# Kernel optimization log

Hardware: AMD Instinct MI355X
Metric: run time of the kernel (lower is better)

Reference implementation:

```python
import jax, jax.numpy as jnp
import numpy as np


def setup_inputs() -> dict:
    key = jax.random.key(0)
    ks = jax.random.split(key, 5)
    b, t, q_dim, kv_dim, h = 16, 128, 256, 64, 4
    c = t - 1
    q_x = jax.random.normal(ks[0], (b, t, q_dim), dtype=jnp.float32)
    kv_x = jax.random.normal(ks[1], (b, t, c, kv_dim), dtype=jnp.float32)
    # Linear weights stored as [in, out]; no biases (bias=False in torch module).
    sq = 1.0 / np.sqrt(q_dim)
    sk = 1.0 / np.sqrt(kv_dim)
    Wq = jax.random.uniform(ks[2], (q_dim, kv_dim * h), jnp.float32, -sq, sq)
    Wk = jax.random.uniform(ks[3], (kv_dim, kv_dim * h), jnp.float32, -sk, sk)
    Wv = jax.random.uniform(ks[4], (kv_dim, kv_dim * h), jnp.float32, -sk, sk)
    return {"q_x": q_x, "kv_x": kv_x, "Wq": Wq, "Wk": Wk, "Wv": Wv}


def reference(q_x, kv_x, Wq, Wk, Wv):
    b, t, c, k = kv_x.shape  # c = t - 1
    h = Wq.shape[1] // k
    # projections
    q = (q_x @ Wq).reshape(b, t, h, k)          # [b,t,h,k]
    keys = (kv_x @ Wk).reshape(b, t, c, h, k)   # [b,t,c,h,k]
    vals = (kv_x @ Wv).reshape(b, t, c, h, k)
    # per-token attention over the c-sized context
    scores = jnp.einsum('bthk,btchk->bthc', q, keys) / jnp.sqrt(jnp.float32(k))
    w = jax.nn.softmax(scores, axis=-1)          # softmax over context dim
    out = jnp.einsum('bthc,btchk->bthk', w, vals)
    return out.reshape(b, t, h * k)
```

## Files before the change

### kernel.cpp

```cpp
#include <hip/hip_runtime.h>
#include <math.h>

#define Bdim 16
#define Tdim 128
#define Cdim 127
#define Hdim 4
#define QD   256
#define HK   256
#define BT   (Bdim * Tdim)

#define DPP_XOR1        0xB1
#define DPP_XOR2        0x4E
#define DPP_HALF_MIRROR 0x141
#define DPP_MIRROR      0x140
template<int CTRL>
__device__ __forceinline__ float dpp_movf(float x) {
    return __int_as_float(__builtin_amdgcn_update_dpp(
        0, __float_as_int(x), CTRL, 0xF, 0xF, true));
}
__device__ __forceinline__ float quad_sum(float v) {
    v += dpp_movf<DPP_XOR1>(v);
    v += dpp_movf<DPP_XOR2>(v);
    return v;
}
__device__ __forceinline__ float rows_sum(float v) {
    v += dpp_movf<DPP_HALF_MIRROR>(v);
    v += dpp_movf<DPP_MIRROR>(v);
    v += __shfl_xor(v, 16, 64);
    v += __shfl_xor(v, 32, 64);
    return v;
}
__device__ __forceinline__ float wx_red(float v) {
    v += dpp_movf<DPP_XOR1>(v);
    v += dpp_movf<DPP_XOR2>(v);
    v += dpp_movf<DPP_HALF_MIRROR>(v);
    v += dpp_movf<DPP_MIRROR>(v);
    v += __shfl_xor(v, 16, 64);
    return v;
}

__global__ __launch_bounds__(256) void qk_fused(
        const float* __restrict__ q_x,
        const float* __restrict__ Wq,
        const float* __restrict__ Wk,
        float* __restrict__ qk) {
    __shared__ __align__(16) float q_s[4][256];
    __shared__ __align__(16) float p_s[4][4][68];
    int RB = blockIdx.x;
    int tid = threadIdx.x;
    {
        int r = tid >> 6, kq = tid & 63;
        *(float4*)&q_s[r][kq*4] =
            *(const float4*)(q_x + (size_t)(RB*4 + r) * QD + kq * 4);
    }
    __syncthreads();

    float acc[4] = {0.f, 0.f, 0.f, 0.f};
    #pragma unroll 4
    for (int i4 = 0; i4 < 64; ++i4) {
        float w0 = Wq[(size_t)(4*i4+0) * HK + tid];
        float w1 = Wq[(size_t)(4*i4+1) * HK + tid];
        float w2 = Wq[(size_t)(4*i4+2) * HK + tid];
        float w3 = Wq[(size_t)(4*i4+3) * HK + tid];
        #pragma unroll
        for (int r = 0; r < 4; ++r) {
            float4 qv = *(const float4*)&q_s[r][i4*4];
            acc[r] = fmaf(qv.x, w0, fmaf(qv.y, w1, fmaf(qv.z, w2, fmaf(qv.w, w3, acc[r]))));
        }
    }
    int h = tid >> 6, m = tid & 63;
    #pragma unroll
    for (int r = 0; r < 4; ++r) p_s[r][h][m] = acc[r];
    __syncthreads();

    const float4* wk4 = (const float4*)(Wk + (size_t)m * HK + h * 64);
    float4 wkr[16];
    #pragma unroll
    for (int j = 0; j < 16; ++j) wkr[j] = wk4[j];
    float a2[4] = {0.f, 0.f, 0.f, 0.f};
    #pragma unroll
    for (int j4 = 0; j4 < 16; ++j4) {
        #pragma unroll
        for (int r = 0; r < 4; ++r) {
            float4 pv = *(const float4*)&p_s[r][h][j4*4];
            a2[r] = fmaf(pv.x, wkr[j4].x, fmaf(pv.y, wkr[j4].y,
                    fmaf(pv.z, wkr[j4].z, fmaf(pv.w, wkr[j4].w, a2[r]))));
        }
    }
    #pragma unroll
    for (int r = 0; r < 4; ++r)
        qk[(size_t)(RB*4 + r) * HK + tid] = a2[r];
}

__global__ __launch_bounds__(512, 8) void attn_main(
        const float* __restrict__ kv_x,
        const float* __restrict__ qk_g,
        const float* __restrict__ Wv,
        float* __restrict__ out) {
    __shared__ __align__(16) float qk_s[HK];
    __shared__ __align__(16) float4 e4[128];
    __shared__ __align__(16) float4 wx4[Hdim * 16];
    __shared__ __align__(16) float4 reds[8];

    int bt  = blockIdx.x;
    int tid = threadIdx.x;
    const float* Xr = kv_x + (size_t)bt * (Cdim * 64);

    if (tid < 256)
        qk_s[tid] = qk_g[(size_t)bt * HK + tid];
    __syncthreads();

    int lane = tid & 63;
    int wave = tid >> 6;
    int c  = tid >> 2;
    int qp = tid & 3;

    float e0, e1, e2, e3;
    {
        bool valid = (c < Cdim);
        int crow = valid ? c : 0;
        const float4* xq = (const float4*)(Xr + crow * 64) + qp * 4;
        float4 x0 = xq[0];
        float4 x1 = xq[1];
        float4 x2 = xq[2];
        float4 x3 = xq[3];
        const float4* qk4 = (const float4*)qk_s;
        float a0 = 0.f, a1 = 0.f, a2 = 0.f, a3 = 0.f;
        #pragma unroll
        for (int i = 0; i < 4; ++i) {
            float4 xi = (i == 0) ? x0 : (i == 1) ? x1 : (i == 2) ? x2 : x3;
            float4 q0 = qk4[0*16 + qp*4 + i];
            float4 q1 = qk4[1*16 + qp*4 + i];
            float4 q2 = qk4[2*16 + qp*4 + i];
            float4 q3 = qk4[3*16 + qp*4 + i];
            a0 = fmaf(q0.x, xi.x, fmaf(q0.y, xi.y, fmaf(q0.z, xi.z, fmaf(q0.w, xi.w, a0))));
            a1 = fmaf(q1.x, xi.x, fmaf(q1.y, xi.y, fmaf(q1.z, xi.z, fmaf(q1.w, xi.w, a1))));
            a2 = fmaf(q2.x, xi.x, fmaf(q2.y, xi.y, fmaf(q2.z, xi.z, fmaf(q2.w, xi.w, a2))));
            a3 = fmaf(q3.x, xi.x, fmaf(q3.y, xi.y, fmaf(q3.z, xi.z, fmaf(q3.w, xi.w, a3))));
        }
        a0 = quad_sum(a0); a1 = quad_sum(a1); a2 = quad_sum(a2); a3 = quad_sum(a3);
        e0 = valid ? __expf(a0 * 0.125f) : 0.f;
        e1 = valid ? __expf(a1 * 0.125f) : 0.f;
        e2 = valid ? __expf(a2 * 0.125f) : 0.f;
        e3 = valid ? __expf(a3 * 0.125f) : 0.f;
    }
    if (qp == 0) e4[c] = make_float4(e0, e1, e2, e3);
    float t0 = rows_sum(e0), t1 = rows_sum(e1), t2 = rows_sum(e2), t3 = rows_sum(e3);
    if (lane == 0) reds[wave] = make_float4(t0, t1, t2, t3);
    __syncthreads();

    {
        int jc = tid >> 5;
        int mq = (lane >> 3) & 3;
        int cs = lane & 7;
        float4 A0 = {0,0,0,0}, A1 = {0,0,0,0}, A2 = {0,0,0,0}, A3 = {0,0,0,0};
        #pragma unroll
        for (int mm = 0; mm < 4; ++mm) {
            int cc = cs + 8 * (mq * 4 + mm);
            int ccrow = (cc < Cdim) ? cc : 0;
            float4 x4 = *(const float4*)(Xr + ccrow * 64 + jc * 4);
            float4 ee = e4[cc];
            A0.x = fmaf(ee.x, x4.x, A0.x); A0.y = fmaf(ee.x, x4.y, A0.y);
            A0.z = fmaf(ee.x, x4.z, A0.z); A0.w = fmaf(ee.x, x4.w, A0.w);
            A1.x = fmaf(ee.y, x4.x, A1.x); A1.y = fmaf(ee.y, x4.y, A1.y);
            A1.z = fmaf(ee.y, x4.z, A1.z); A1.w = fmaf(ee.y, x4.w, A1.w);
            A2.x = fmaf(ee.z, x4.x, A2.x); A2.y = fmaf(ee.z, x4.y, A2.y);
            A2.z = fmaf(ee.z, x4.z, A2.z); A2.w = fmaf(ee.z, x4.w, A2.w);
            A3.x = fmaf(ee.w, x4.x, A3.x); A3.y = fmaf(ee.w, x4.y, A3.y);
            A3.z = fmaf(ee.w, x4.z, A3.z); A3.w = fmaf(ee.w, x4.w, A3.w);
        }
        A0.x = wx_red(A0.x); A0.y = wx_red(A0.y); A0.z = wx_red(A0.z); A0.w = wx_red(A0.w);
        A1.x = wx_red(A1.x); A1.y = wx_red(A1.y); A1.z = wx_red(A1.z); A1.w = wx_red(A1.w);
        A2.x = wx_red(A2.x); A2.y = wx_red(A2.y); A2.z = wx_red(A2.z); A2.w = wx_red(A2.w);
        A3.x = wx_red(A3.x); A3.y = wx_red(A3.y); A3.z = wx_red(A3.z); A3.w = wx_red(A3.w);
        if ((lane & 31) == 0) {
            wx4[0 * 16 + jc] = A0;
            wx4[1 * 16 + jc] = A1;
            wx4[2 * 16 + jc] = A2;
            wx4[3 * 16 + jc] = A3;
        }
    }
    __syncthreads();

    if (tid < 256) {
        int hh = tid >> 6, k = tid & 63;
        float4 sums = reds[0];
        #pragma unroll
        for (int w = 1; w < 8; ++w) {
            float4 r = reds[w];
            sums.x += r.x; sums.y += r.y; sums.z += r.z; sums.w += r.w;
        }
        float denom = (hh == 0) ? sums.x : (hh == 1) ? sums.y
                    : (hh == 2) ? sums.z : sums.w;
        float inv = 1.f / denom;
        const float* wvcol = Wv + hh * 64 + k;
        float acc = 0.f;
        #pragma unroll 4
        for (int jc = 0; jc < 16; ++jc) {
            float4 w4 = wx4[hh * 16 + jc];
            acc = fmaf(w4.x, wvcol[(size_t)(jc*4+0) * HK],
                  fmaf(w4.y, wvcol[(size_t)(jc*4+1) * HK],
                  fmaf(w4.z, wvcol[(size_t)(jc*4+2) * HK],
                  fmaf(w4.w, wvcol[(size_t)(jc*4+3) * HK], acc))));
        }
        out[(size_t)bt * HK + tid] = acc * inv;
    }
}

extern "C" void kernel_launch(void* const* d_in, const int* in_sizes, int n_in,
                              void* d_out, int out_size, void* d_ws, size_t ws_size,
                              hipStream_t stream) {
    const float* q_x  = (const float*)d_in[0];
    const float* kv_x = (const float*)d_in[1];
    const float* Wq   = (const float*)d_in[2];
    const float* Wk   = (const float*)d_in[3];
    const float* Wv   = (const float*)d_in[4];
    float* out = (float*)d_out;

    float* qk = (float*)d_ws;

    qk_fused<<<BT / 4, 256, 0, stream>>>(q_x, Wq, Wk, qk);
    attn_main<<<BT, 512, 0, stream>>>(kv_x, qk, Wv, out);
}
```

Baseline: 42.76 us.

## Split attention into one-wave-per-token core kernel and separate batched V projection

```diff
diff --git a/kernel.cpp b/kernel.cpp
--- a/kernel.cpp
+++ b/kernel.cpp
@@ -18,24 +18,13 @@
     return __int_as_float(__builtin_amdgcn_update_dpp(
         0, __float_as_int(x), CTRL, 0xF, 0xF, true));
 }
-__device__ __forceinline__ float quad_sum(float v) {
-    v += dpp_movf<DPP_XOR1>(v);
-    v += dpp_movf<DPP_XOR2>(v);
-    return v;
-}
-__device__ __forceinline__ float rows_sum(float v) {
-    v += dpp_movf<DPP_HALF_MIRROR>(v);
-    v += dpp_movf<DPP_MIRROR>(v);
-    v += __shfl_xor(v, 16, 64);
-    v += __shfl_xor(v, 32, 64);
-    return v;
-}
-__device__ __forceinline__ float wx_red(float v) {
+__device__ __forceinline__ float sum64(float v) {
     v += dpp_movf<DPP_XOR1>(v);
     v += dpp_movf<DPP_XOR2>(v);
     v += dpp_movf<DPP_HALF_MIRROR>(v);
     v += dpp_movf<DPP_MIRROR>(v);
     v += __shfl_xor(v, 16, 64);
+    v += __shfl_xor(v, 32, 64);
     return v;
 }
 
@@ -92,74 +81,71 @@
         qk[(size_t)(RB*4 + r) * HK + tid] = a2[r];
 }
 
-__global__ __launch_bounds__(512, 8) void attn_main(
+__global__ __launch_bounds__(256) void attn_core(
         const float* __restrict__ kv_x,
         const float* __restrict__ qk_g,
-        const float* __restrict__ Wv,
-        float* __restrict__ out) {
-    __shared__ __align__(16) float qk_s[HK];
-    __shared__ __align__(16) float4 e4[128];
-    __shared__ __align__(16) float4 wx4[Hdim * 16];
-    __shared__ __align__(16) float4 reds[8];
-
-    int bt  = blockIdx.x;
+        float* __restrict__ wx_buf,
+        float* __restrict__ denom_buf) {
+    __shared__ __align__(16) float4 qk_s[4][64];
+    __shared__ __align__(16) float4 e4[4][128];
+
     int tid = threadIdx.x;
+    int wv = tid >> 6, lane = tid & 63;
+    int bt = blockIdx.x * 4 + wv;
     const float* Xr = kv_x + (size_t)bt * (Cdim * 64);
 
-    if (tid < 256)
-        qk_s[tid] = qk_g[(size_t)bt * HK + tid];
-    __syncthreads();
-
-    int lane = tid & 63;
-    int wave = tid >> 6;
-    int c  = tid >> 2;
-    int qp = tid & 3;
-
-    float e0, e1, e2, e3;
+    qk_s[wv][lane] = ((const float4*)(qk_g + (size_t)bt * HK))[lane];
+
+    const float4* xA = (const float4*)(Xr + lane * 64);
+    int cB = 64 + lane;
+    bool vB = (cB < Cdim);
+    const float4* xB = (const float4*)(Xr + (vB ? cB : 0) * 64);
+    float a0=0.f,a1=0.f,a2=0.f,a3=0.f;
+    float b0=0.f,b1=0.f,b2=0.f,b3=0.f;
+    #pragma unroll
+    for (int i = 0; i < 16; ++i) {
+        float4 xa = xA[i];
+        float4 xb = xB[i];
+        float4 q0 = qk_s[wv][ 0 + i];
+        float4 q1 = qk_s[wv][16 + i];
+        float4 q2 = qk_s[wv][32 + i];
+        float4 q3 = qk_s[wv][48 + i];
+        a0 = fmaf(q0.x, xa.x, fmaf(q0.y, xa.y, fmaf(q0.z, xa.z, fmaf(q0.w, xa.w, a0))));
+        a1 = fmaf(q1.x, xa.x, fmaf(q1.y, xa.y, fmaf(q1.z, xa.z, fmaf(q1.w, xa.w, a1))));
+        a2 = fmaf(q2.x, xa.x, fmaf(q2.y, xa.y, fmaf(q2.z, xa.z, fmaf(q2.w, xa.w, a2))));
+        a3 = fmaf(q3.x, xa.x, fmaf(q3.y, xa.y, fmaf(q3.z, xa.z, fmaf(q3.w, xa.w, a3))));
+        b0 = fmaf(q0.x, xb.x, fmaf(q0.y, xb.y, fmaf(q0.z, xb.z, fmaf(q0.w, xb.w, b0))));
+        b1 = fmaf(q1.x, xb.x, fmaf(q1.y, xb.y, fmaf(q1.z, xb.z, fmaf(q1.w, xb.w, b1))));
+        b2 = fmaf(q2.x, xb.x, fmaf(q2.y, xb.y, fmaf(q2.z, xb.z, fmaf(q2.w, xb.w, b2))));
+        b3 = fmaf(q3.x, xb.x, fmaf(q3.y, xb.y, fmaf(q3.z, xb.z, fmaf(q3.w, xb.w, b3))));
+    }
+
+    float4 eA, eB;
+    eA.x = __expf(a0 * 0.125f);  eA.y = __expf(a1 * 0.125f);
+    eA.z = __expf(a2 * 0.125f);  eA.w = __expf(a3 * 0.125f);
+    eB.x = vB ? __expf(b0 * 0.125f) : 0.f;
+    eB.y = vB ? __expf(b1 * 0.125f) : 0.f;
+    eB.z = vB ? __expf(b2 * 0.125f) : 0.f;
+    eB.w = vB ? __expf(b3 * 0.125f) : 0.f;
+    e4[wv][lane]      = eA;
+    e4[wv][64 + lane] = eB;
+
+    float t0 = sum64(eA.x + eB.x);
+    float t1 = sum64(eA.y + eB.y);
+    float t2 = sum64(eA.z + eB.z);
+    float t3 = sum64(eA.w + eB.w);
+    if (lane == 0)
+        *(float4*)(denom_buf + (size_t)bt * 4) = make_float4(t0, t1, t2, t3);
+
     {
-        bool valid = (c < Cdim);
-        int crow = valid ? c : 0;
-        const float4* xq = (const float4*)(Xr + crow * 64) + qp * 4;
-        float4 x0 = xq[0];
-        float4 x1 = xq[1];
-        float4 x2 = xq[2];
-        float4 x3 = xq[3];
-        const float4* qk4 = (const float4*)qk_s;
-        float a0 = 0.f, a1 = 0.f, a2 = 0.f, a3 = 0.f;
-        #pragma unroll
-        for (int i = 0; i < 4; ++i) {
-            float4 xi = (i == 0) ? x0 : (i == 1) ? x1 : (i == 2) ? x2 : x3;
-            float4 q0 = qk4[0*16 + qp*4 + i];
-            float4 q1 = qk4[1*16 + qp*4 + i];
-            float4 q2 = qk4[2*16 + qp*4 + i];
-            float4 q3 = qk4[3*16 + qp*4 + i];
-            a0 = fmaf(q0.x, xi.x, fmaf(q0.y, xi.y, fmaf(q0.z, xi.z, fmaf(q0.w, xi.w, a0))));
-            a1 = fmaf(q1.x, xi.x, fmaf(q1.y, xi.y, fmaf(q1.z, xi.z, fmaf(q1.w, xi.w, a1))));
-            a2 = fmaf(q2.x, xi.x, fmaf(q2.y, xi.y, fmaf(q2.z, xi.z, fmaf(q2.w, xi.w, a2))));
-            a3 = fmaf(q3.x, xi.x, fmaf(q3.y, xi.y, fmaf(q3.z, xi.z, fmaf(q3.w, xi.w, a3))));
-        }
-        a0 = quad_sum(a0); a1 = quad_sum(a1); a2 = quad_sum(a2); a3 = quad_sum(a3);
-        e0 = valid ? __expf(a0 * 0.125f) : 0.f;
-        e1 = valid ? __expf(a1 * 0.125f) : 0.f;
-        e2 = valid ? __expf(a2 * 0.125f) : 0.f;
-        e3 = valid ? __expf(a3 * 0.125f) : 0.f;
-    }
-    if (qp == 0) e4[c] = make_float4(e0, e1, e2, e3);
-    float t0 = rows_sum(e0), t1 = rows_sum(e1), t2 = rows_sum(e2), t3 = rows_sum(e3);
-    if (lane == 0) reds[wave] = make_float4(t0, t1, t2, t3);
-    __syncthreads();
-
-    {
-        int jc = tid >> 5;
-        int mq = (lane >> 3) & 3;
-        int cs = lane & 7;
+        int jc = lane >> 2, g = lane & 3;
         float4 A0 = {0,0,0,0}, A1 = {0,0,0,0}, A2 = {0,0,0,0}, A3 = {0,0,0,0};
-        #pragma unroll
-        for (int mm = 0; mm < 4; ++mm) {
-            int cc = cs + 8 * (mq * 4 + mm);
-            int ccrow = (cc < Cdim) ? cc : 0;
-            float4 x4 = *(const float4*)(Xr + ccrow * 64 + jc * 4);
-            float4 ee = e4[cc];
+        #pragma unroll 8
+        for (int mm = 0; mm < 32; ++mm) {
+            int cc = g + 4 * mm;
+            int crow = (cc < Cdim) ? cc : 0;
+            float4 x4 = *(const float4*)(Xr + crow * 64 + jc * 4);
+            float4 ee = e4[wv][cc];
             A0.x = fmaf(ee.x, x4.x, A0.x); A0.y = fmaf(ee.x, x4.y, A0.y);
             A0.z = fmaf(ee.x, x4.z, A0.z); A0.w = fmaf(ee.x, x4.w, A0.w);
             A1.x = fmaf(ee.y, x4.x, A1.x); A1.y = fmaf(ee.y, x4.y, A1.y);
@@ -169,41 +155,54 @@
             A3.x = fmaf(ee.w, x4.x, A3.x); A3.y = fmaf(ee.w, x4.y, A3.y);
             A3.z = fmaf(ee.w, x4.z, A3.z); A3.w = fmaf(ee.w, x4.w, A3.w);
         }
-        A0.x = wx_red(A0.x); A0.y = wx_red(A0.y); A0.z = wx_red(A0.z); A0.w = wx_red(A0.w);
-        A1.x = wx_red(A1.x); A1.y = wx_red(A1.y); A1.z = wx_red(A1.z); A1.w = wx_red(A1.w);
-        A2.x = wx_red(A2.x); A2.y = wx_red(A2.y); A2.z = wx_red(A2.z); A2.w = wx_red(A2.w);
-        A3.x = wx_red(A3.x); A3.y = wx_red(A3.y); A3.z = wx_red(A3.z); A3.w = wx_red(A3.w);
-        if ((lane & 31) == 0) {
-            wx4[0 * 16 + jc] = A0;
-            wx4[1 * 16 + jc] = A1;
-            wx4[2 * 16 + jc] = A2;
-            wx4[3 * 16 + jc] = A3;
-        }
-    }
+        #define GRED(v) v += dpp_movf<DPP_XOR1>(v); v += dpp_movf<DPP_XOR2>(v);
+        GRED(A0.x) GRED(A0.y) GRED(A0.z) GRED(A0.w)
+        GRED(A1.x) GRED(A1.y) GRED(A1.z) GRED(A1.w)
+        GRED(A2.x) GRED(A2.y) GRED(A2.z) GRED(A2.w)
+        GRED(A3.x) GRED(A3.y) GRED(A3.z) GRED(A3.w)
+        #undef GRED
+        if (g == 0) {
+            float4* w = (float4*)(wx_buf + (size_t)bt * HK);
+            w[0 * 16 + jc] = A0;
+            w[1 * 16 + jc] = A1;
+            w[2 * 16 + jc] = A2;
+            w[3 * 16 + jc] = A3;
+        }
+    }
+}
+
+__global__ __launch_bounds__(256) void vproj(
+        const float* __restrict__ wx_buf,
+        const float* __restrict__ denom_buf,
+        const float* __restrict__ Wv,
+        float* __restrict__ out) {
+    __shared__ __align__(16) float4 wx_s[4][64];
+    __shared__ __align__(16) float4 dn_s[4];
+    int B0 = blockIdx.x * 4;
+    int tid = threadIdx.x;
+    {
+        int r = tid >> 6, l = tid & 63;
+        wx_s[r][l] = ((const float4*)(wx_buf + (size_t)(B0 + r) * HK))[l];
+    }
+    if (tid < 4) dn_s[tid] = *(const float4*)(denom_buf + (size_t)(B0 + tid) * 4);
     __syncthreads();
 
-    if (tid < 256) {
-        int hh = tid >> 6, k = tid & 63;
-        float4 sums = reds[0];
+    int h = tid >> 6;
+    float wvr[64];
+    #pragma unroll
+    for (int j = 0; j < 64; ++j) wvr[j] = Wv[(size_t)j * HK + tid];
+    #pragma unroll
+    for (int r = 0; r < 4; ++r) {
+        float acc = 0.f;
         #pragma unroll
-        for (int w = 1; w < 8; ++w) {
-            float4 r = reds[w];
-            sums.x += r.x; sums.y += r.y; sums.z += r.z; sums.w += r.w;
-        }
-        float denom = (hh == 0) ? sums.x : (hh == 1) ? sums.y
-                    : (hh == 2) ? sums.z : sums.w;
-        float inv = 1.f / denom;
-        const float* wvcol = Wv + hh * 64 + k;
-        float acc = 0.f;
-        #pragma unroll 4
-        for (int jc = 0; jc < 16; ++jc) {
-            float4 w4 = wx4[hh * 16 + jc];
-            acc = fmaf(w4.x, wvcol[(size_t)(jc*4+0) * HK],
-                  fmaf(w4.y, wvcol[(size_t)(jc*4+1) * HK],
-                  fmaf(w4.z, wvcol[(size_t)(jc*4+2) * HK],
-                  fmaf(w4.w, wvcol[(size_t)(jc*4+3) * HK], acc))));
-        }
-        out[(size_t)bt * HK + tid] = acc * inv;
+        for (int j4 = 0; j4 < 16; ++j4) {
+            float4 w4 = wx_s[r][h * 16 + j4];
+            acc = fmaf(w4.x, wvr[j4*4+0], fmaf(w4.y, wvr[j4*4+1],
+                  fmaf(w4.z, wvr[j4*4+2], fmaf(w4.w, wvr[j4*4+3], acc))));
+        }
+        float4 dn = dn_s[r];
+        float d = (h == 0) ? dn.x : (h == 1) ? dn.y : (h == 2) ? dn.z : dn.w;
+        out[(size_t)(B0 + r) * HK + tid] = acc / d;
     }
 }
 
@@ -217,8 +216,11 @@
     const float* Wv   = (const float*)d_in[4];
     float* out = (float*)d_out;
 
-    float* qk = (float*)d_ws;
-
-    qk_fused<<<BT / 4, 256, 0, stream>>>(q_x, Wq, Wk, qk);
-    attn_main<<<BT, 512, 0, stream>>>(kv_x, qk, Wv, out);
-}
+    float* qk    = (float*)d_ws;
+    float* wxb   = qk + (size_t)BT * HK;
+    float* denom = wxb + (size_t)BT * HK;
+
+    qk_fused <<<BT / 4, 256, 0, stream>>>(q_x, Wq, Wk, qk);
+    attn_core<<<BT / 4, 256, 0, stream>>>(kv_x, qk, wxb, denom);
+    vproj    <<<BT / 4, 256, 0, stream>>>(wxb, denom, Wv, out);
+}
```

Result: slower. 74.36 us (+73.9%).
